# Optimization experiments

Measured on AMD Instinct MI355X. Metric: run time of the kernel, lower is better.

The kernel has to match this reference:

```python
import jax, jax.numpy as jnp
import numpy as np

NQ = 8
N = 2 ** NQ
NCYC = 4
B = 8192
_POP = np.array([bin(i).count('1') for i in range(N)], dtype=np.float32)  # popcount per basis state
_CNOT = np.array([[1, 0, 0, 0], [0, 1, 0, 0], [0, 0, 0, 1], [0, 0, 1, 0]], dtype=np.complex64)
_I4 = np.eye(4, dtype=np.complex64)
_XX = np.fliplr(np.eye(4)).astype(np.complex64)  # X (x) X in the 2-qubit basis


def _apply1(psi, U, w):
    # single-qubit gate U (2x2) on wire w; psi: (B, 256)
    b = psi.shape[0]
    s = psi.reshape(b, 1 << w, 2, -1)
    return jnp.einsum('ij,bljr->blir', U, s).reshape(b, N)


def _apply2_adj_b(psi, U, w):
    # batched 4x4 gate U (B,4,4) on adjacent wires (w, w+1)
    b = psi.shape[0]
    s = psi.reshape(b, 1 << w, 4, -1)
    return jnp.einsum('bij,bljr->blir', U, s).reshape(b, N)


def _apply2(psi, U, w0, w1):
    # fixed 4x4 gate on arbitrary wires (w0, w1)
    b = psi.shape[0]
    t = psi.reshape((b,) + (2,) * NQ)
    t = jnp.tensordot(jnp.asarray(U).reshape(2, 2, 2, 2), t, axes=((2, 3), (w0 + 1, w1 + 1)))
    t = jnp.moveaxis(t, (0, 1), (w0 + 1, w1 + 1))
    return t.reshape(b, N)


def _rz_mat(t):
    e = jnp.exp(-0.5j * t)
    return jnp.diag(jnp.stack([e, jnp.conj(e)])).astype(jnp.complex64)


def _ry_mat(t):
    c = jnp.cos(0.5 * t)
    s = jnp.sin(0.5 * t)
    return jnp.stack([jnp.stack([c, -s]), jnp.stack([s, c])]).astype(jnp.complex64)


def _u3_mat(p):
    th, ph, la = p[0], p[1], p[2]
    cc = jnp.cos(0.5 * th).astype(jnp.complex64)
    ss = jnp.sin(0.5 * th).astype(jnp.complex64)
    r0 = jnp.stack([cc, -jnp.exp(1j * la) * ss])
    r1 = jnp.stack([jnp.exp(1j * ph) * ss, jnp.exp(1j * (ph + la)) * cc])
    return jnp.stack([r0, r1]).astype(jnp.complex64)


def _expz(psi, w):
    # <Z_w> = p(bit=0) - p(bit=1)
    b = psi.shape[0]
    p = jnp.abs(psi.reshape(b, 1 << w, 2, -1)) ** 2
    m = p.sum(axis=(1, 3))
    return m[:, 0] - m[:, 1]


def _conv(psi, rz3, ry2, wq, wp):
    # RZ(wq) CNOT(wq,wp) RZ(wp) RY(wq) CNOT(wp,wq) RY(wq) CNOT(wq,wp) RZ(wp)
    psi = _apply1(psi, _rz_mat(rz3[0]), wq)
    psi = _apply2(psi, _CNOT, wq, wp)
    psi = _apply1(psi, _rz_mat(rz3[1]), wp)
    psi = _apply1(psi, _ry_mat(ry2[0]), wq)
    psi = _apply2(psi, _CNOT, wp, wq)
    psi = _apply1(psi, _ry_mat(ry2[1]), wq)
    psi = _apply2(psi, _CNOT, wq, wp)
    psi = _apply1(psi, _rz_mat(rz3[2]), wp)
    return psi


def setup_inputs() -> dict:
    key = jax.random.key(0)
    ks = jax.random.split(key, 8)
    pi = np.float32(np.pi)
    theta = jax.random.uniform(ks[0], (B,), jnp.float32, 0.0, pi / 2)
    phi = jax.random.uniform(ks[1], (B,), jnp.float32, 0.0, pi / 2)
    rz_params = jax.random.uniform(ks[2], (21,), jnp.float32, -pi, pi)
    ry_params = jax.random.uniform(ks[3], (14,), jnp.float32, -pi, pi)
    u3_params = jax.random.uniform(ks[4], (6, 3), jnp.float32, -pi, pi)
    w1 = jax.random.normal(ks[5], (10, 2), jnp.float32) / np.sqrt(2.0).astype(np.float32)
    b1 = jnp.zeros((10,), jnp.float32)
    w2 = jax.random.normal(ks[6], (1, 10), jnp.float32) / np.sqrt(10.0).astype(np.float32)
    b2 = jnp.zeros((1,), jnp.float32)
    return {'theta': theta, 'phi': phi, 'rz_params': rz_params, 'ry_params': ry_params,
            'u3_params': u3_params, 'w1': w1, 'b1': b1, 'w2': w2, 'b2': b2}


def reference(theta, phi, rz_params, ry_params, u3_params, w1, b1, w2, b2):
    b = theta.shape[0]
    # H on every wire from |0...0> -> uniform amplitudes 1/sqrt(2^8)
    psi = jnp.full((b, N), np.float32(2.0 ** (-NQ / 2)), dtype=jnp.complex64)
    # rz(2*phi) on all 8 wires == diagonal phase exp(i*phi*(2*popcount - 8))
    zphase = jnp.exp(1j * phi[:, None] * (2.0 * _POP[None, :] - NQ)).astype(jnp.complex64)
    # rxx(2*theta): cos(theta) I - i sin(theta) XX, batched over angles
    c = jnp.cos(theta)
    s = jnp.sin(theta)
    Urxx = (c[:, None, None] * _I4 - 1j * s[:, None, None] * _XX).astype(jnp.complex64)
    for _ in range(NCYC):
        psi = psi * zphase
        for w in (0, 2, 4, 6):  # pairs (0,1),(2,3),(4,5),(6,7)
            psi = _apply2_adj_b(psi, Urxx, w)
        for w in (1, 3, 5):  # pairs (1,2),(3,4),(5,6)
            psi = _apply2_adj_b(psi, Urxx, w)
    # first conv layer on pairs (1,0),(3,2),(5,4),(7,6)
    for i, (wq, wp) in enumerate([(1, 0), (3, 2), (5, 4), (7, 6)]):
        psi = _conv(psi, rz_params[3 * i:3 * i + 3], ry_params[2 * i:2 * i + 2], wq, wp)
    # U3 pooling on wires 1,3,5,7
    for i, w in enumerate((1, 3, 5, 7)):
        psi = _apply1(psi, _u3_mat(u3_params[i]), w)
    # second conv layer on pairs (3,1),(7,5),(5,3)
    for j, (wq, wp) in enumerate([(3, 1), (7, 5), (5, 3)]):
        i = 4 + j
        psi = _conv(psi, rz_params[3 * i:3 * i + 3], ry_params[2 * i:2 * i + 2], wq, wp)
    psi = _apply1(psi, _u3_mat(u3_params[4]), 3)
    psi = _apply1(psi, _u3_mat(u3_params[5]), 7)
    feats = jnp.stack([_expz(psi, 3), _expz(psi, 7)], axis=-1)  # (B, 2)
    h = jnp.tanh(feats @ w1.T + b1)
    return jax.nn.sigmoid(h @ w2.T + b2)  # (B, 1)
```

## Files before the change

### kernel.cpp

```cpp
#include <hip/hip_runtime.h>

typedef float f32x2 __attribute__((ext_vector_type(2)));
typedef f32x2 cplx;

__device__ __forceinline__ cplx pk_bcastlo_mul(cplx a, cplx b){
  cplx t;
  asm("v_pk_mul_f32 %0, %1, %2 op_sel:[0,0] op_sel_hi:[0,1]"
      : "=v"(t) : "v"(a), "v"(b));
  return t;
}
__device__ __forceinline__ cplx pk_cross_mad(cplx a, cplx b, cplx t){
  cplx d;
  asm("v_pk_fma_f32 %0, %1, %2, %3 op_sel:[1,1,0] op_sel_hi:[1,0,1] neg_lo:[0,1,0]"
      : "=v"(d) : "v"(a), "v"(b), "v"(t));
  return d;
}
__device__ __forceinline__ cplx pk_bcastlo_mad(cplx a, cplx b, cplx acc){
  cplx t;
  asm("v_pk_fma_f32 %0, %1, %2, %3 op_sel:[0,0,0] op_sel_hi:[0,1,1]"
      : "=v"(t) : "v"(a), "v"(b), "v"(acc));
  return t;
}
__device__ __forceinline__ cplx pk_rxx_cross(cplx cs, cplx p, cplx t){
  cplx d;
  asm("v_pk_fma_f32 %0, %1, %2, %3 op_sel:[1,1,0] op_sel_hi:[1,0,1] neg_hi:[0,1,0]"
      : "=v"(d) : "v"(cs), "v"(p), "v"(t));
  return d;
}

__device__ __forceinline__ cplx cmul(cplx a, cplx b){
  return pk_cross_mad(a, b, pk_bcastlo_mul(a, b));
}
__device__ __forceinline__ cplx cmad(cplx a, cplx b, cplx acc){
  return pk_cross_mad(a, b, pk_bcastlo_mad(a, b, acc));
}
__device__ __forceinline__ cplx rxx_upd(cplx cs, cplx a, cplx p){
  return pk_rxx_cross(cs, p, pk_bcastlo_mul(cs, a));
}

__device__ __forceinline__ void rz_gate(cplx* st, float t, int bmask){
  float s, c; sincosf(0.5f*t, &s, &c);
  cplx em = {c, -s}, ep = {c, s};
  for(int k=0;k<4;k++) st[k] = cmul(st[k], (k & bmask) ? ep : em);
}
__device__ __forceinline__ void ry_gate_q(cplx* st, float t){
  float s, c; sincosf(0.5f*t, &s, &c);
  for(int bp=0;bp<2;bp++){
    cplx a0 = st[bp], a1 = st[2+bp];
    st[bp]   = c*a0 - s*a1;
    st[2+bp] = s*a0 + c*a1;
  }
}
__device__ __forceinline__ void u3_gate(cplx* st, const float* p, int onq){
  float th=p[0], ph=p[1], la=p[2];
  float ss,cc,sl,cl,sp,cp,spl,cpl;
  sincosf(0.5f*th,&ss,&cc); sincosf(la,&sl,&cl); sincosf(ph,&sp,&cp); sincosf(ph+la,&spl,&cpl);
  cplx u00={cc,0.f},      u01={-cl*ss,-sl*ss};
  cplx u10={cp*ss,sp*ss}, u11={cpl*cc,spl*cc};
  if(onq){
    for(int bp=0;bp<2;bp++){
      cplx a0=st[bp], a1=st[2+bp];
      st[bp]   = cmad(u01,a1,cmul(u00,a0));
      st[2+bp] = cmad(u11,a1,cmul(u10,a0));
    }
  } else {
    for(int bq=0;bq<2;bq++){
      cplx a0=st[2*bq], a1=st[2*bq+1];
      st[2*bq]   = cmad(u01,a1,cmul(u00,a0));
      st[2*bq+1] = cmad(u11,a1,cmul(u10,a0));
    }
  }
}


#define DPP_XOR1 0xB1
#define DPP_XOR2 0x4E
#define DPP_XOR3 0x1B
#define DPP_ROR8 0x128
#define DPP_MIRR 0x140
#define DPP_HALF 0x141

template<int C>
__device__ __forceinline__ float xdpp(float x){
  return __builtin_bit_cast(float,
    __builtin_amdgcn_mov_dpp(__builtin_bit_cast(int, x), C, 0xF, 0xF, true));
}

enum Sh { SH_DPP1, SH_DPP2, SH_DPP3, SH_ROR8, SH_SWZ4, SH_SWZ6, SH_SWZ10, SH_SWZ12 };

template<Sh S> __device__ __forceinline__ float shf(float x){
  if      constexpr(S==SH_DPP1)  return xdpp<DPP_XOR1>(x);
  else if constexpr(S==SH_DPP2)  return xdpp<DPP_XOR2>(x);
  else if constexpr(S==SH_DPP3)  return xdpp<DPP_XOR3>(x);
  else if constexpr(S==SH_ROR8)  return xdpp<DPP_ROR8>(x);
  else if constexpr(S==SH_SWZ4)  return xdpp<DPP_HALF>(xdpp<DPP_XOR3>(x));
  else if constexpr(S==SH_SWZ6)  return xdpp<DPP_HALF>(xdpp<DPP_XOR1>(x));
  else if constexpr(S==SH_SWZ10) return xdpp<DPP_ROR8>(xdpp<DPP_XOR2>(x));
  else                           return xdpp<DPP_MIRR>(xdpp<DPP_XOR3>(x));
}
template<Sh S> __device__ __forceinline__ cplx shc(cplx a){
  cplx r; r[0] = shf<S>(a[0]); r[1] = shf<S>(a[1]); return r;
}

template<int MR>
__device__ __forceinline__ void rxx_reg(cplx* v, cplx cs){
  #pragma unroll
  for(int r=0;r<16;r++){
    int q = r ^ MR;
    if(r > q) continue;
    cplx a = v[r], b = v[q];
    v[r] = rxx_upd(cs, a, b);
    v[q] = rxx_upd(cs, b, a);
  }
}
template<Sh S>
__device__ __forceinline__ void rxx_lane(cplx* v, cplx cs){
  #pragma unroll
  for(int r=0;r<16;r++){
    cplx p = shc<S>(v[r]);
    v[r] = rxx_upd(cs, v[r], p);
  }
}
__device__ __forceinline__ void rxx_mix34(cplx* v, cplx cs){
  #pragma unroll
  for(int r=0;r<16;r+=2){
    cplx pa = shc<SH_DPP1>(v[r^1]);
    cplx pb = shc<SH_DPP1>(v[r]);
    cplx a = v[r], b = v[r^1];
    v[r]   = rxx_upd(cs, a, pa);
    v[r^1] = rxx_upd(cs, b, pb);
  }
}

template<int MQ, int MP>
__device__ __forceinline__ void conv_reg(cplx* v, const cplx* M){
  #pragma unroll
  for(int r=0;r<16;r++){
    if((r & (MQ|MP)) != 0) continue;
    cplx a0=v[r], a1=v[r^MP], a2=v[r^MQ], a3=v[r^MQ^MP];
    v[r]        = cmad(M[3], a3, cmad(M[2], a2, cmad(M[1], a1, cmul(M[0], a0))));
    v[r^MP]     = cmad(M[7], a3, cmad(M[6], a2, cmad(M[5], a1, cmul(M[4], a0))));
    v[r^MQ]     = cmad(M[11],a3, cmad(M[10],a2, cmad(M[9], a1, cmul(M[8], a0))));
    v[r^MQ^MP]  = cmad(M[15],a3, cmad(M[14],a2, cmad(M[13],a1, cmul(M[12],a0))));
  }
}

template<Sh SQ, Sh SP, Sh SB>
__device__ __forceinline__ void conv_lane(cplx* v, const cplx* M, int k){
  cplx es = M[k*4 + k], ep = M[k*4 + (k^1)], eq = M[k*4 + (k^2)], eb = M[k*4 + (k^3)];
  #pragma unroll
  for(int r=0;r<16;r++){
    cplx pq = shc<SQ>(v[r]);
    cplx pp = shc<SP>(v[r]);
    cplx pb = shc<SB>(v[r]);
    v[r] = cmad(eb, pb, cmad(eq, pq, cmad(ep, pp, cmul(es, v[r]))));
  }
}

__device__ __forceinline__ void conv_53(cplx* v, const cplx* M, int s1){
  int t = 2*s1, u = 2 - t;
  const cplx* r0 = M + t*4;
  const cplx* r1 = M + (t+1)*4;
  cplx e00=r0[t], e01=r0[t+1], e02=r0[u], e03=r0[u+1];
  cplx e10=r1[t], e11=r1[t+1], e12=r1[u], e13=r1[u+1];
  #pragma unroll
  for(int r=0;r<16;r+=2){
    cplx pv0 = shc<SH_DPP2>(v[r]);
    cplx pv1 = shc<SH_DPP2>(v[r+1]);
    cplx a0 = v[r], a1 = v[r+1];
    v[r]   = cmad(e03, pv1, cmad(e02, pv0, cmad(e01, a1, cmul(e00, a0))));
    v[r+1] = cmad(e13, pv1, cmad(e12, pv0, cmad(e11, a1, cmul(e10, a0))));
  }
}

__global__ void __launch_bounds__(256) qcnn_kernel(
    const float* __restrict__ theta, const float* __restrict__ phi,
    const float* __restrict__ rz, const float* __restrict__ ry,
    const float* __restrict__ u3,
    const float* __restrict__ w1, const float* __restrict__ b1,
    const float* __restrict__ w2, const float* __restrict__ b2,
    float* __restrict__ out){
  __shared__ cplx Msh[112];

  int tid  = threadIdx.x;

  if(tid < 28){
    int ci = tid >> 2, col = tid & 3;
    const float* rz3 = rz + 3*ci;
    const float* ry2 = ry + 2*ci;
    int u3slot = 0, u3idx = 0;
    if(ci <= 3){ u3slot = 1; u3idx = ci; }
    else if(ci == 5){ u3slot = 1; u3idx = 5; }
    else if(ci == 6){ u3slot = 2; u3idx = 4; }
    cplx st[4];
    for(int k=0;k<4;k++){ cplx z = {k==col ? 1.f : 0.f, 0.f}; st[k] = z; }
    rz_gate(st, rz3[0], 2);
    { cplx tmp=st[2]; st[2]=st[3]; st[3]=tmp; }
    rz_gate(st, rz3[1], 1);
    ry_gate_q(st, ry2[0]);
    { cplx tmp=st[1]; st[1]=st[3]; st[3]=tmp; }
    ry_gate_q(st, ry2[1]);
    { cplx tmp=st[2]; st[2]=st[3]; st[3]=tmp; }
    rz_gate(st, rz3[2], 1);
    if(u3slot == 1)      u3_gate(st, u3+3*u3idx, 1);
    else if(u3slot == 2) u3_gate(st, u3+3*u3idx, 0);
    for(int k=0;k<4;k++) Msh[ci*16 + k*4 + col] = st[k];
  }
  __syncthreads();

  int s_   = tid & 15;
  int b    = blockIdx.x*16 + (tid >> 4);
  int s0 = s_&1, s1 = (s_>>1)&1, s2 = (s_>>2)&1, s3 = (s_>>3)&1;
  (void)s2;

  float th = theta[b], ph = phi[b];
  float c, s;
  __sincosf(th, &s, &c);
  cplx cs = {c, s};

  cplx zp[5];
  {
    int base = __popc(s_);
    float a0 = ph * (float)(2*base - 8);
    float sa, ca, s2p, c2p;
    __sincosf(a0, &sa, &ca);
    __sincosf(2.f*ph, &s2p, &c2p);
    cplx step = {c2p, s2p};
    cplx z0 = {ca, sa};
    zp[0] = z0;
    #pragma unroll
    for(int j=1;j<5;j++) zp[j] = cmul(zp[j-1], step);
  }

  cplx v[16];
  #pragma unroll
  for(int r=0;r<16;r++) v[r] = 0.0625f * zp[__popc(r)];

  #pragma unroll 1
  for(int cyc=0;cyc<4;cyc++){
    if(cyc){
      #pragma unroll
      for(int r=0;r<16;r++) v[r] = cmul(v[r], zp[__popc(r)]);
    }
    rxx_reg<12>(v, cs);
    rxx_reg<3>(v, cs);
    rxx_lane<SH_DPP3>(v, cs);
    rxx_lane<SH_SWZ12>(v, cs);
    rxx_reg<6>(v, cs);
    rxx_mix34(v, cs);
    rxx_lane<SH_SWZ6>(v, cs);
  }

  conv_reg<4,8>(v, Msh +  0);
  conv_reg<1,2>(v, Msh + 16);
  conv_lane<SH_DPP2,SH_DPP1,SH_DPP3>(v, Msh + 32, 2*s1 + s0);
  conv_lane<SH_ROR8,SH_SWZ4,SH_SWZ12>(v, Msh + 48, 2*s3 + s2);
  conv_reg<1,4>(v, Msh + 64);
  conv_lane<SH_ROR8,SH_DPP2,SH_SWZ10>(v, Msh + 80, 2*s3 + s1);
  conv_53(v, Msh + 96, s1);

  float tot = 0.f, z3 = 0.f;
  #pragma unroll
  for(int r=0;r<16;r++){
    float m = fmaf(v[r][0], v[r][0], v[r][1]*v[r][1]);
    tot += m;
    z3 += (r & 1) ? -m : m;
  }
  float z7 = (s_ & 8) ? -tot : tot;
  z3 += xdpp<DPP_XOR1>(z3);  z7 += xdpp<DPP_XOR1>(z7);
  z3 += xdpp<DPP_XOR2>(z3);  z7 += xdpp<DPP_XOR2>(z7);
  z3 += xdpp<DPP_HALF>(z3);  z7 += xdpp<DPP_HALF>(z7);
  z3 += xdpp<DPP_ROR8>(z3);  z7 += xdpp<DPP_ROR8>(z7);

  float acc = 0.f;
  if(s_ < 10){
    float hv = tanhf(z3*w1[2*s_] + z7*w1[2*s_+1] + b1[s_]);
    acc = hv * w2[s_];
  }
  acc += xdpp<DPP_XOR1>(acc);
  acc += xdpp<DPP_XOR2>(acc);
  acc += xdpp<DPP_HALF>(acc);
  acc += xdpp<DPP_ROR8>(acc);

  if(s_ == 0){
    float a = acc + b2[0];
    out[b] = 1.f / (1.f + __expf(-a));
  }
}

extern "C" void kernel_launch(void* const* d_in, const int* in_sizes, int n_in,
                              void* d_out, int out_size, void* d_ws, size_t ws_size,
                              hipStream_t stream) {
  const float* theta = (const float*)d_in[0];
  const float* phi   = (const float*)d_in[1];
  const float* rz    = (const float*)d_in[2];
  const float* ry    = (const float*)d_in[3];
  const float* u3    = (const float*)d_in[4];
  const float* w1    = (const float*)d_in[5];
  const float* b1    = (const float*)d_in[6];
  const float* w2    = (const float*)d_in[7];
  const float* b2    = (const float*)d_in[8];

  hipLaunchKernelGGL(qcnn_kernel, dim3(8192/16), dim3(256), 0, stream,
                     theta, phi, rz, ry, u3, w1, b1, w2, b2, (float*)d_out);
}
```

Baseline: 85.05 us.

## Remap lane-to-qubit encoding so RXX lane exchanges use single DPP ops

Changes how the four lane-resident qubit bits map onto lane index bits, using XOR-combined bits (b4=s0^s2, b6=s2^s3). Under this mapping the per-cycle RXX lane exchanges need only a single DPP move each (xor3, ror8, half-mirror) instead of two chained DPPs. The cost is that some one-off conv layers now need chained shuffles, and the popcount phase and conv index selection are updated to match. The hot loop runs four cycles, so cutting DPP instructions there is meant to lower instruction count and latency.

Measured after the change: 84.68 us. About the same (-0.4%).

```diff
diff --git a/kernel.cpp b/kernel.cpp
--- a/kernel.cpp
+++ b/kernel.cpp
@@ -86,17 +86,17 @@
     __builtin_amdgcn_mov_dpp(__builtin_bit_cast(int, x), C, 0xF, 0xF, true));
 }
 
-enum Sh { SH_DPP1, SH_DPP2, SH_DPP3, SH_ROR8, SH_SWZ4, SH_SWZ6, SH_SWZ10, SH_SWZ12 };
+enum Sh { SH_X1, SH_X2, SH_X3, SH_R8, SH_HALF, SH_MIRR, SH_M5, SH_M13 };
 
 template<Sh S> __device__ __forceinline__ float shf(float x){
-  if      constexpr(S==SH_DPP1)  return xdpp<DPP_XOR1>(x);
-  else if constexpr(S==SH_DPP2)  return xdpp<DPP_XOR2>(x);
-  else if constexpr(S==SH_DPP3)  return xdpp<DPP_XOR3>(x);
-  else if constexpr(S==SH_ROR8)  return xdpp<DPP_ROR8>(x);
-  else if constexpr(S==SH_SWZ4)  return xdpp<DPP_HALF>(xdpp<DPP_XOR3>(x));
-  else if constexpr(S==SH_SWZ6)  return xdpp<DPP_HALF>(xdpp<DPP_XOR1>(x));
-  else if constexpr(S==SH_SWZ10) return xdpp<DPP_ROR8>(xdpp<DPP_XOR2>(x));
-  else                           return xdpp<DPP_MIRR>(xdpp<DPP_XOR3>(x));
+  if      constexpr(S==SH_X1)   return xdpp<DPP_XOR1>(x);
+  else if constexpr(S==SH_X2)   return xdpp<DPP_XOR2>(x);
+  else if constexpr(S==SH_X3)   return xdpp<DPP_XOR3>(x);
+  else if constexpr(S==SH_R8)   return xdpp<DPP_ROR8>(x);
+  else if constexpr(S==SH_HALF) return xdpp<DPP_HALF>(x);
+  else if constexpr(S==SH_MIRR) return xdpp<DPP_MIRR>(x);
+  else if constexpr(S==SH_M5)   return xdpp<DPP_HALF>(xdpp<DPP_XOR2>(x));
+  else                          return xdpp<DPP_MIRR>(xdpp<DPP_XOR2>(x));
 }
 template<Sh S> __device__ __forceinline__ cplx shc(cplx a){
   cplx r; r[0] = shf<S>(a[0]); r[1] = shf<S>(a[1]); return r;
@@ -124,8 +124,8 @@
 __device__ __forceinline__ void rxx_mix34(cplx* v, cplx cs){
   #pragma unroll
   for(int r=0;r<16;r+=2){
-    cplx pa = shc<SH_DPP1>(v[r^1]);
-    cplx pb = shc<SH_DPP1>(v[r]);
+    cplx pa = shc<SH_X1>(v[r^1]);
+    cplx pb = shc<SH_X1>(v[r]);
     cplx a = v[r], b = v[r^1];
     v[r]   = rxx_upd(cs, a, pa);
     v[r^1] = rxx_upd(cs, b, pb);
@@ -157,16 +157,16 @@
   }
 }
 
-__device__ __forceinline__ void conv_53(cplx* v, const cplx* M, int s1){
-  int t = 2*s1, u = 2 - t;
+__device__ __forceinline__ void conv_53(cplx* v, const cplx* M, int b5){
+  int t = 2*b5, u = 2 - t;
   const cplx* r0 = M + t*4;
   const cplx* r1 = M + (t+1)*4;
   cplx e00=r0[t], e01=r0[t+1], e02=r0[u], e03=r0[u+1];
   cplx e10=r1[t], e11=r1[t+1], e12=r1[u], e13=r1[u+1];
   #pragma unroll
   for(int r=0;r<16;r+=2){
-    cplx pv0 = shc<SH_DPP2>(v[r]);
-    cplx pv1 = shc<SH_DPP2>(v[r+1]);
+    cplx pv0 = shc<SH_X2>(v[r]);
+    cplx pv1 = shc<SH_X2>(v[r+1]);
     cplx a0 = v[r], a1 = v[r+1];
     v[r]   = cmad(e03, pv1, cmad(e02, pv0, cmad(e01, a1, cmul(e00, a0))));
     v[r+1] = cmad(e13, pv1, cmad(e12, pv0, cmad(e11, a1, cmul(e10, a0))));
@@ -211,7 +211,7 @@
   int s_   = tid & 15;
   int b    = blockIdx.x*16 + (tid >> 4);
   int s0 = s_&1, s1 = (s_>>1)&1, s2 = (s_>>2)&1, s3 = (s_>>3)&1;
-  (void)s2;
+  int b4 = s0 ^ s2, b5 = s1, b6 = s2 ^ s3, b7 = s3;
 
   float th = theta[b], ph = phi[b];
   float c, s;
@@ -220,7 +220,7 @@
 
   cplx zp[5];
   {
-    int base = __popc(s_);
+    int base = b4 + b5 + b6 + b7;
     float a0 = ph * (float)(2*base - 8);
     float sa, ca, s2p, c2p;
     __sincosf(a0, &sa, &ca);
@@ -244,20 +244,20 @@
     }
     rxx_reg<12>(v, cs);
     rxx_reg<3>(v, cs);
-    rxx_lane<SH_DPP3>(v, cs);
-    rxx_lane<SH_SWZ12>(v, cs);
+    rxx_lane<SH_X3>(v, cs);
+    rxx_lane<SH_R8>(v, cs);
     rxx_reg<6>(v, cs);
     rxx_mix34(v, cs);
-    rxx_lane<SH_SWZ6>(v, cs);
+    rxx_lane<SH_HALF>(v, cs);
   }
 
   conv_reg<4,8>(v, Msh +  0);
   conv_reg<1,2>(v, Msh + 16);
-  conv_lane<SH_DPP2,SH_DPP1,SH_DPP3>(v, Msh + 32, 2*s1 + s0);
-  conv_lane<SH_ROR8,SH_SWZ4,SH_SWZ12>(v, Msh + 48, 2*s3 + s2);
+  conv_lane<SH_X2,SH_X1,SH_X3>(Msh ? v : v, Msh + 32, 2*b5 + b4);
+  conv_lane<SH_M13,SH_M5,SH_R8>(v, Msh + 48, 2*b7 + b6);
   conv_reg<1,4>(v, Msh + 64);
-  conv_lane<SH_ROR8,SH_DPP2,SH_SWZ10>(v, Msh + 80, 2*s3 + s1);
-  conv_53(v, Msh + 96, s1);
+  conv_lane<SH_M13,SH_X2,SH_MIRR>(v, Msh + 80, 2*b7 + b5);
+  conv_53(v, Msh + 96, b5);
 
   float tot = 0.f, z3 = 0.f;
   #pragma unroll
@@ -266,7 +266,7 @@
     tot += m;
     z3 += (r & 1) ? -m : m;
   }
-  float z7 = (s_ & 8) ? -tot : tot;
+  float z7 = b7 ? -tot : tot;
   z3 += xdpp<DPP_XOR1>(z3);  z7 += xdpp<DPP_XOR1>(z7);
   z3 += xdpp<DPP_XOR2>(z3);  z7 += xdpp<DPP_XOR2>(z7);
   z3 += xdpp<DPP_HALF>(z3);  z7 += xdpp<DPP_HALF>(z7);
```
